# Kernel optimization log

Measured on AMD Instinct MI355X. Metric: run time of the kernel, lower is better.

## Reference

```python
import jax, jax.numpy as jnp
import numpy as np

D_MODEL = 512
NHEAD = 8
HEAD_DIM = D_MODEL // NHEAD  # 64
ROTARY_DIM = HEAD_DIM        # rotary_dim defaults to head_dim
WINDOW = (127, 128)          # (left, right) sliding window, flash-attn convention
ROPE_BASE = 10000.0


def setup_inputs() -> dict:
    key = jax.random.key(0)
    k1, k2, k3, k4 = jax.random.split(key, 4)
    N, T = 4, 2048
    x = jax.random.normal(k1, (N, T, D_MODEL), dtype=jnp.float32)
    # Wqkv: Linear(d_model, 3*d_model, bias=False) -> weight [3*D, D]
    Wqkv_w = jax.random.normal(k2, (3 * D_MODEL, D_MODEL), dtype=jnp.float32) * (D_MODEL ** -0.5)
    # out_proj: Linear(d_model, d_model, bias=True)
    out_w = jax.random.normal(k3, (D_MODEL, D_MODEL), dtype=jnp.float32) * (D_MODEL ** -0.5)
    out_b = jax.random.normal(k4, (D_MODEL,), dtype=jnp.float32) * 0.01
    return {"x": x, "Wqkv_w": Wqkv_w, "out_w": out_w, "out_b": out_b}


def _rope_cos_sin(T, dtype):
    # flash-attn RotaryEmbedding: inv_freq over even indices of rotary_dim
    inv_freq = 1.0 / (ROPE_BASE ** (jnp.arange(0, ROTARY_DIM, 2, dtype=jnp.float32) / ROTARY_DIM))
    t = jnp.arange(T, dtype=jnp.float32)
    freqs = jnp.outer(t, inv_freq)  # [T, ROTARY_DIM//2]
    return jnp.cos(freqs).astype(dtype), jnp.sin(freqs).astype(dtype)


def _apply_rotary(x, cos, sin):
    # non-interleaved (rotate halves); x: [N, T, H, hd], rotary over first ROTARY_DIM dims
    r, rest = x[..., :ROTARY_DIM], x[..., ROTARY_DIM:]
    half = ROTARY_DIM // 2
    x1, x2 = r[..., :half], r[..., half:]
    c = cos[None, :, None, :]  # [1, T, 1, half]
    s = sin[None, :, None, :]
    rotated = jnp.concatenate([x1 * c - x2 * s, x2 * c + x1 * s], axis=-1)
    return jnp.concatenate([rotated, rest], axis=-1) if rest.shape[-1] else rotated


def reference(x, Wqkv_w, out_w, out_b):
    N, T, D = x.shape
    qkv = jnp.einsum('ntd,ed->nte', x, Wqkv_w).reshape(N, T, 3, NHEAD, HEAD_DIM)
    q, k, v = qkv[:, :, 0], qkv[:, :, 1], qkv[:, :, 2]  # each [N, T, H, hd]
    cos, sin = _rope_cos_sin(T, x.dtype)
    q = _apply_rotary(q, cos, sin)
    k = _apply_rotary(k, cos, sin)
    scale = HEAD_DIM ** -0.5
    scores = jnp.einsum('nthd,nshd->nhts', q, k) * scale  # [N, H, T, T]
    # sliding window: query i attends key j iff i - left <= j <= i + right
    i = jnp.arange(T)[:, None]
    j = jnp.arange(T)[None, :]
    mask = (j >= i - WINDOW[0]) & (j <= i + WINDOW[1])  # [T, T]
    scores = jnp.where(mask[None, None], scores, jnp.finfo(scores.dtype).min)
    attn = jax.nn.softmax(scores, axis=-1)
    ctx = jnp.einsum('nhts,nshd->nthd', attn, v).reshape(N, T, D)
    return jnp.einsum('ntd,ed->nte', ctx, out_w) + out_b
```

## Files before the change

kernel.cpp:

```cpp
#include <hip/hip_runtime.h>
#include <math.h>

#define TSEQ 2048
#define NB 4
#define DM 512
#define NH 8
#define HD 64

typedef _Float16 half8 __attribute__((ext_vector_type(8)));
typedef _Float16 half4 __attribute__((ext_vector_type(4)));
typedef float floatx4 __attribute__((ext_vector_type(4)));


#define WS_END_U16 2916352

__global__ void prep(const float* __restrict__ x, const float* __restrict__ wqkv,
                     const float* __restrict__ ow, char* __restrict__ ws) {
  for (int i = blockIdx.x * 256 + threadIdx.x; i < WS_END_U16; i += 2048 * 256) {
    if (i < 524288) {
      const float4 a = ((const float4*)x)[2 * i];
      const float4 b = ((const float4*)x)[2 * i + 1];
      half8 h;
      h[0] = (_Float16)a.x; h[1] = (_Float16)a.y; h[2] = (_Float16)a.z; h[3] = (_Float16)a.w;
      h[4] = (_Float16)b.x; h[5] = (_Float16)b.y; h[6] = (_Float16)b.z; h[7] = (_Float16)b.w;
      *(half8*)(ws + (size_t)i * 16) = h;
    } else if (i >= 540672 && i < 638976) {
      const int o = i - 540672;
      const float4 a = ((const float4*)wqkv)[2 * o];
      const float4 b = ((const float4*)wqkv)[2 * o + 1];
      half8 h;
      h[0] = (_Float16)a.x; h[1] = (_Float16)a.y; h[2] = (_Float16)a.z; h[3] = (_Float16)a.w;
      h[4] = (_Float16)b.x; h[5] = (_Float16)b.y; h[6] = (_Float16)b.z; h[7] = (_Float16)b.w;
      *(half8*)(ws + (size_t)i * 16) = h;
    } else if (i >= 655360 && i < 688128) {
      const int o = i - 655360;
      const float4 a = ((const float4*)ow)[2 * o];
      const float4 b = ((const float4*)ow)[2 * o + 1];
      half8 h;
      h[0] = (_Float16)a.x; h[1] = (_Float16)a.y; h[2] = (_Float16)a.z; h[3] = (_Float16)a.w;
      h[4] = (_Float16)b.x; h[5] = (_Float16)b.y; h[6] = (_Float16)b.z; h[7] = (_Float16)b.w;
      *(half8*)(ws + (size_t)i * 16) = h;
    } else if (i >= 2883584) {
      const int u = i - 2883584;
      float4 o4;
      {
        const int id = 2 * u, t = id >> 5, fi = id & 31;
        const float invf = powf(10000.0f, -(float)(2 * fi) * (1.0f / 64.0f));
        float s, c; sincosf((float)t * invf, &s, &c);
        o4.x = c; o4.y = s;
      }
      {
        const int id = 2 * u + 1, t = id >> 5, fi = id & 31;
        const float invf = powf(10000.0f, -(float)(2 * fi) * (1.0f / 64.0f));
        float s, c; sincosf((float)t * invf, &s, &c);
        o4.z = c; o4.w = s;
      }
      ((float4*)(ws + 46137344))[u] = o4;
    } else {
      ((float4*)ws)[i] = make_float4(0.f, 0.f, 0.f, 0.f);
    }
  }
}

__global__ __launch_bounds__(256) void qkv_gemm_mfma(
    const _Float16* __restrict__ A, const _Float16* __restrict__ B,
    const float2* __restrict__ rope,
    _Float16* __restrict__ qb, _Float16* __restrict__ kb, _Float16* __restrict__ vT)
{
  __shared__ _Float16 As[128 * 40];
  __shared__ _Float16 Bs[128 * 40];
  const int tid = threadIdx.x;
  const int wv = tid >> 6, lane = tid & 63, quad = lane >> 4, col = lane & 15;
  const int wm = wv >> 1, we = wv & 1;
  const int m0 = blockIdx.x << 7, c0 = blockIdx.y << 7;
  const int sr = tid >> 1, sc = (tid & 1) << 4;
  const _Float16* ap = &A[(size_t)(m0 + sr) * DM + sc];
  const _Float16* bp = &B[(size_t)(c0 + sr) * DM + sc];
  floatx4 acc[4][4] = {};
  for (int k0 = 0; k0 < DM; k0 += 32) {
    const half8 a0 = *(const half8*)(ap + k0);
    const half8 a1 = *(const half8*)(ap + k0 + 8);
    const half8 b0 = *(const half8*)(bp + k0);
    const half8 b1 = *(const half8*)(bp + k0 + 8);
    __syncthreads();
    *(half8*)&As[sr * 40 + sc] = a0;
    *(half8*)&As[sr * 40 + sc + 8] = a1;
    *(half8*)&Bs[sr * 40 + sc] = b0;
    *(half8*)&Bs[sr * 40 + sc + 8] = b1;
    __syncthreads();
    half8 af[4], bf[4];
#pragma unroll
    for (int mt = 0; mt < 4; mt++)
      af[mt] = *(const half8*)&As[(wm * 64 + mt * 16 + col) * 40 + quad * 8];
#pragma unroll
    for (int et = 0; et < 4; et++)
      bf[et] = *(const half8*)&Bs[(we * 64 + et * 16 + col) * 40 + quad * 8];
#pragma unroll
    for (int mt = 0; mt < 4; mt++)
#pragma unroll
      for (int et = 0; et < 4; et++)
        acc[mt][et] = __builtin_amdgcn_mfma_f32_16x16x32_f16(af[mt], bf[et], acc[mt][et], 0, 0, 0);
  }
  const int eidx = (c0 >> 6) + we;
  const int three = eidx >> 3, h = eidx & 7;
  const int mbase = m0 + wm * 64 + quad * 4;
  if (three == 2) {
#pragma unroll
    for (int mt = 0; mt < 4; mt++) {
      const int m = mbase + mt * 16;
      const int n = m >> 11, t = m & 2047;
#pragma unroll
      for (int et = 0; et < 4; et++) {
        const int dh = et * 16 + col;
        half4 hv;
#pragma unroll
        for (int r = 0; r < 4; r++) hv[r] = (_Float16)acc[mt][et][r];
        *(half4*)&vT[(size_t)(n * NH + h) * HD * TSEQ + (size_t)dh * TSEQ + t] = hv;
      }
    }
  } else {
    _Float16* dst = three ? kb : qb;
    const float scl = three ? 1.0f : 0.125f;
#pragma unroll
    for (int mt = 0; mt < 4; mt++)
#pragma unroll
      for (int r = 0; r < 4; r++) {
        const int m = mbase + mt * 16 + r;
        const int n = m >> 11, t = m & 2047;
#pragma unroll
        for (int et = 0; et < 4; et++) {
          const int i = ((et & 1) << 4) + col;
          const float2 cs = rope[t * 32 + i];
          const float v = acc[mt][et][r];
          const float v2 = acc[mt][et ^ 2][r];
          const float o = (et < 2) ? (v * cs.x - v2 * cs.y) : (v * cs.x + v2 * cs.y);
          dst[((size_t)(n * NH + h) * TSEQ + t) * HD + et * 16 + col] = (_Float16)(o * scl);
        }
      }
  }
}

__global__ __launch_bounds__(256, 4) void attn_win_mfma(
    const _Float16* __restrict__ qb, const _Float16* __restrict__ kb,
    const _Float16* __restrict__ vT, _Float16* __restrict__ ctx)
{
  __shared__ __align__(16) char smem[36864];
  _Float16* Ks = (_Float16*)smem;
  _Float16* Vt = (_Float16*)(smem + 9216);
  _Float16* Ps = (_Float16*)(smem + 18432);
  _Float16* Osh = (_Float16*)(smem + 27648);

  const int tid = threadIdx.x;
  const int wv = tid >> 6;
  const int lane = tid & 63;
  const int quad = lane >> 4;
  const int col = lane & 15;
  const int nh = blockIdx.y;
  const int q0 = blockIdx.x << 6;
  const _Float16* qp = qb + (size_t)nh * TSEQ * HD;
  const _Float16* kp = kb + (size_t)nh * TSEQ * HD;
  const _Float16* vp = vT + (size_t)nh * HD * TSEQ;

  const int i_row = (wv << 4) + col;
  const int ig = q0 + i_row;
  const half8 qf0 = *(const half8*)&qp[(size_t)ig * HD + (quad << 3)];
  const half8 qf1 = *(const half8*)&qp[(size_t)ig * HD + 32 + (quad << 3)];

  float m_i = -1e30f, l_i = 0.0f;
  floatx4 accO[4] = {};

  const int kt0 = max(0, q0 - 127) >> 6;
  const int kt1 = min(TSEQ - 1, q0 + 191) >> 6;
  const int kr = tid >> 2, kc = (tid & 3) << 4;
  const int vd = tid >> 2, vc = (tid & 3) << 4;
  for (int kt = kt0; kt <= kt1; kt++) {
    const int j0 = kt << 6;
    const half8 k0_ = *(const half8*)&kp[(size_t)(j0 + kr) * HD + kc];
    const half8 k1_ = *(const half8*)&kp[(size_t)(j0 + kr) * HD + kc + 8];
    const half8 v0_ = *(const half8*)&vp[(size_t)vd * TSEQ + j0 + vc];
    const half8 v1_ = *(const half8*)&vp[(size_t)vd * TSEQ + j0 + vc + 8];
    __syncthreads();
    *(half8*)&Ks[kr * 72 + kc] = k0_;
    *(half8*)&Ks[kr * 72 + kc + 8] = k1_;
    *(half8*)&Vt[vd * 72 + vc] = v0_;
    *(half8*)&Vt[vd * 72 + vc + 8] = v1_;
    __syncthreads();

    floatx4 S[4];
#pragma unroll
    for (int js = 0; js < 4; js++) {
      const half8 a0 = *(const half8*)&Ks[((js << 4) + col) * 72 + (quad << 3)];
      const half8 a1 = *(const half8*)&Ks[((js << 4) + col) * 72 + 32 + (quad << 3)];
      floatx4 c = {0.f, 0.f, 0.f, 0.f};
      c = __builtin_amdgcn_mfma_f32_16x16x32_f16(a0, qf0, c, 0, 0, 0);
      c = __builtin_amdgcn_mfma_f32_16x16x32_f16(a1, qf1, c, 0, 0, 0);
      S[js] = c;
    }
    float mx = -1e30f;
#pragma unroll
    for (int js = 0; js < 4; js++)
#pragma unroll
      for (int r = 0; r < 4; r++) {
        const int jg = j0 + (js << 4) + (quad << 2) + r;
        const bool valid = (jg >= ig - 127) && (jg <= ig + 128);
        const float s = valid ? S[js][r] : -INFINITY;
        S[js][r] = s;
        mx = fmaxf(mx, s);
      }
    mx = fmaxf(mx, __shfl_xor(mx, 16, 64));
    mx = fmaxf(mx, __shfl_xor(mx, 32, 64));
    const float m_new = fmaxf(m_i, mx);
    const float alpha = __expf(m_i - m_new);
    float lsum = 0.f;
#pragma unroll
    for (int js = 0; js < 4; js++) {
      half4 ph;
#pragma unroll
      for (int r = 0; r < 4; r++) {
        const float p = __expf(S[js][r] - m_new);
        lsum += p;
        ph[r] = (_Float16)p;
      }
      *(half4*)&Ps[i_row * 72 + (js << 4) + (quad << 2)] = ph;
    }
    lsum += __shfl_xor(lsum, 16, 64);
    lsum += __shfl_xor(lsum, 32, 64);
    l_i = l_i * alpha + lsum;
    m_i = m_new;
    float a4[4];
#pragma unroll
    for (int r = 0; r < 4; r++) a4[r] = __shfl(alpha, (quad << 2) + r, 64);
#pragma unroll
    for (int d4 = 0; d4 < 4; d4++)
#pragma unroll
      for (int r = 0; r < 4; r++) accO[d4][r] *= a4[r];
    __syncthreads();
    const half8 pa0 = *(const half8*)&Ps[i_row * 72 + (quad << 3)];
    const half8 pa1 = *(const half8*)&Ps[i_row * 72 + 32 + (quad << 3)];
#pragma unroll
    for (int d4 = 0; d4 < 4; d4++) {
      const half8 vb0 = *(const half8*)&Vt[((d4 << 4) + col) * 72 + (quad << 3)];
      const half8 vb1 = *(const half8*)&Vt[((d4 << 4) + col) * 72 + 32 + (quad << 3)];
      accO[d4] = __builtin_amdgcn_mfma_f32_16x16x32_f16(pa0, vb0, accO[d4], 0, 0, 0);
      accO[d4] = __builtin_amdgcn_mfma_f32_16x16x32_f16(pa1, vb1, accO[d4], 0, 0, 0);
    }
  }
  {
    const float linv = 1.0f / l_i;
    float l4[4];
#pragma unroll
    for (int r = 0; r < 4; r++) l4[r] = __shfl(linv, (quad << 2) + r, 64);
#pragma unroll
    for (int d4 = 0; d4 < 4; d4++)
#pragma unroll
      for (int r = 0; r < 4; r++)
        Osh[((wv << 4) + (quad << 2) + r) * 72 + (d4 << 4) + col] = (_Float16)(accO[d4][r] * l4[r]);
  }
  __syncthreads();
  {
    const int n = nh >> 3, h = nh & 7;
    const int oi = tid >> 2, oc = (tid & 3) << 4;
    _Float16* dst = &ctx[((size_t)n * TSEQ + q0 + oi) * DM + h * HD + oc];
    *(half8*)&dst[0] = *(const half8*)&Osh[oi * 72 + oc];
    *(half8*)&dst[8] = *(const half8*)&Osh[oi * 72 + oc + 8];
  }
}

__global__ __launch_bounds__(256) void out_gemm_mfma(
    const _Float16* __restrict__ A, const _Float16* __restrict__ B,
    const float* __restrict__ bias, float* __restrict__ out)
{
  __shared__ _Float16 As[128 * 40];
  __shared__ _Float16 Bs[64 * 40];
  const int tid = threadIdx.x;
  const int wv = tid >> 6, lane = tid & 63, quad = lane >> 4, col = lane & 15;
  const int wm = wv >> 1, we = wv & 1;
  const int m0 = blockIdx.x << 7, c0 = blockIdx.y << 6;
  const int sr = tid >> 1, sc = (tid & 1) << 4;
  const int br = tid >> 2, bc = (tid & 3) << 3;
  const _Float16* ap = &A[(size_t)(m0 + sr) * DM + sc];
  const _Float16* bp = &B[(size_t)(c0 + br) * DM + bc];
  floatx4 acc[4][2] = {};
  for (int k0 = 0; k0 < DM; k0 += 32) {
    const half8 a0 = *(const half8*)(ap + k0);
    const half8 a1 = *(const half8*)(ap + k0 + 8);
    const half8 b0 = *(const half8*)(bp + k0);
    __syncthreads();
    *(half8*)&As[sr * 40 + sc] = a0;
    *(half8*)&As[sr * 40 + sc + 8] = a1;
    *(half8*)&Bs[br * 40 + bc] = b0;
    __syncthreads();
    half8 af[4], bf[2];
#pragma unroll
    for (int mt = 0; mt < 4; mt++)
      af[mt] = *(const half8*)&As[(wm * 64 + mt * 16 + col) * 40 + quad * 8];
#pragma unroll
    for (int et = 0; et < 2; et++)
      bf[et] = *(const half8*)&Bs[(we * 32 + et * 16 + col) * 40 + quad * 8];
#pragma unroll
    for (int mt = 0; mt < 4; mt++)
#pragma unroll
      for (int et = 0; et < 2; et++)
        acc[mt][et] = __builtin_amdgcn_mfma_f32_16x16x32_f16(af[mt], bf[et], acc[mt][et], 0, 0, 0);
  }
  float bb[2];
#pragma unroll
  for (int et = 0; et < 2; et++) bb[et] = bias[c0 + we * 32 + et * 16 + col];
  const int mbase = m0 + wm * 64 + quad * 4;
#pragma unroll
  for (int mt = 0; mt < 4; mt++)
#pragma unroll
    for (int r = 0; r < 4; r++) {
      const int m = mbase + mt * 16 + r;
#pragma unroll
      for (int et = 0; et < 2; et++)
        out[(size_t)m * DM + c0 + we * 32 + et * 16 + col] = acc[mt][et][r] + bb[et];
    }
}

extern "C" void kernel_launch(void* const* d_in, const int* in_sizes, int n_in,
                              void* d_out, int out_size, void* d_ws, size_t ws_size,
                              hipStream_t stream) {
  const float* x    = (const float*)d_in[0];
  const float* wqkv = (const float*)d_in[1];
  const float* ow   = (const float*)d_in[2];
  const float* ob   = (const float*)d_in[3];
  char* ws = (char*)d_ws;
  _Float16* xh    = (_Float16*)(ws);
  _Float16* wqkvh = (_Float16*)(ws + 8650752);
  _Float16* owh   = (_Float16*)(ws + 10485760);
  _Float16* qbuf  = (_Float16*)(ws + 11534336);
  _Float16* kbuf  = (_Float16*)(ws + 20971520);
  _Float16* vTb   = (_Float16*)(ws + 29360128);
  _Float16* ctxh  = (_Float16*)(ws + 37748736);
  float2*   rope  = (float2*)  (ws + 46137344);

  prep<<<2048, 256, 0, stream>>>(x, wqkv, ow, ws);
  qkv_gemm_mfma<<<dim3(64, 12), 256, 0, stream>>>(xh, wqkvh, rope, qbuf, kbuf, vTb);
  attn_win_mfma<<<dim3(32, 32), 256, 0, stream>>>(qbuf, kbuf, vTb, ctxh);
  out_gemm_mfma<<<dim3(64, 8), 256, 0, stream>>>(ctxh, owh, ob, (float*)d_out);
}
```

Before: 139.2 us.

## Use 128-wide key tiles with fixed three-iteration loop in windowed attention

The attention kernel now processes keys in 128-wide tiles aligned to 128, always looping over three tiles with clamped loads, instead of 64-wide tiles spanning the window. This halves the number of barrier-separated iterations and online-softmax rescales, and drops the barrier between P writes and P reads because each wave reads only its own rows. In exchange LDS grows to 52KB, occupancy bound drops to 3 blocks, and aligned tiles cover more masked-out keys than before.

```diff
diff --git a/kernel.cpp b/kernel.cpp
--- a/kernel.cpp
+++ b/kernel.cpp
@@ -140,15 +140,15 @@
   }
 }
 
-__global__ __launch_bounds__(256, 4) void attn_win_mfma(
+__global__ __launch_bounds__(256, 3) void attn_win_mfma(
     const _Float16* __restrict__ qb, const _Float16* __restrict__ kb,
     const _Float16* __restrict__ vT, _Float16* __restrict__ ctx)
 {
-  __shared__ __align__(16) char smem[36864];
+  __shared__ __align__(16) char smem[53248];
   _Float16* Ks = (_Float16*)smem;
-  _Float16* Vt = (_Float16*)(smem + 9216);
-  _Float16* Ps = (_Float16*)(smem + 18432);
-  _Float16* Osh = (_Float16*)(smem + 27648);
+  _Float16* Vt = (_Float16*)(smem + 18432);
+  _Float16* Ps = (_Float16*)(smem + 35840);
+  _Float16* Osh = (_Float16*)smem;
 
   const int tid = threadIdx.x;
   const int wv = tid >> 6;
@@ -169,26 +169,34 @@
   float m_i = -1e30f, l_i = 0.0f;
   floatx4 accO[4] = {};
 
-  const int kt0 = max(0, q0 - 127) >> 6;
-  const int kt1 = min(TSEQ - 1, q0 + 191) >> 6;
-  const int kr = tid >> 2, kc = (tid & 3) << 4;
-  const int vd = tid >> 2, vc = (tid & 3) << 4;
-  for (int kt = kt0; kt <= kt1; kt++) {
-    const int j0 = kt << 6;
-    const half8 k0_ = *(const half8*)&kp[(size_t)(j0 + kr) * HD + kc];
-    const half8 k1_ = *(const half8*)&kp[(size_t)(j0 + kr) * HD + kc + 8];
-    const half8 v0_ = *(const half8*)&vp[(size_t)vd * TSEQ + j0 + vc];
-    const half8 v1_ = *(const half8*)&vp[(size_t)vd * TSEQ + j0 + vc + 8];
-    __syncthreads();
-    *(half8*)&Ks[kr * 72 + kc] = k0_;
-    *(half8*)&Ks[kr * 72 + kc + 8] = k1_;
-    *(half8*)&Vt[vd * 72 + vc] = v0_;
-    *(half8*)&Vt[vd * 72 + vc + 8] = v1_;
-    __syncthreads();
-
-    floatx4 S[4];
-#pragma unroll
-    for (int js = 0; js < 4; js++) {
+  const int kr = tid >> 1, kc = (tid & 1) << 5;
+  const int vd = tid >> 2, vc = (tid & 3) << 5;
+  const int jb0 = (q0 & ~127) - 128;
+  for (int it = 0; it < 3; it++) {
+    const int jb = jb0 + (it << 7);
+    if (jb + 128 <= 0 || jb >= TSEQ) continue;
+    const int jrc = min(max(jb + kr, 0), TSEQ - 1);
+    half8 kreg[4], vreg[4];
+#pragma unroll
+    for (int c = 0; c < 4; c++)
+      kreg[c] = *(const half8*)&kp[(size_t)jrc * HD + kc + (c << 3)];
+#pragma unroll
+    for (int c = 0; c < 4; c++) {
+      const int jv = min(max(jb + vc + (c << 3), 0), TSEQ - 8);
+      vreg[c] = *(const half8*)&vp[(size_t)vd * TSEQ + jv];
+    }
+    __syncthreads();
+#pragma unroll
+    for (int c = 0; c < 4; c++)
+      *(half8*)&Ks[kr * 72 + kc + (c << 3)] = kreg[c];
+#pragma unroll
+    for (int c = 0; c < 4; c++)
+      *(half8*)&Vt[vd * 136 + vc + (c << 3)] = vreg[c];
+    __syncthreads();
+
+    floatx4 S[8];
+#pragma unroll
+    for (int js = 0; js < 8; js++) {
       const half8 a0 = *(const half8*)&Ks[((js << 4) + col) * 72 + (quad << 3)];
       const half8 a1 = *(const half8*)&Ks[((js << 4) + col) * 72 + 32 + (quad << 3)];
       floatx4 c = {0.f, 0.f, 0.f, 0.f};
@@ -196,14 +204,14 @@
       c = __builtin_amdgcn_mfma_f32_16x16x32_f16(a1, qf1, c, 0, 0, 0);
       S[js] = c;
     }
+    const int lo = max(ig - 127, 0), hi = min(ig + 128, TSEQ - 1);
     float mx = -1e30f;
 #pragma unroll
-    for (int js = 0; js < 4; js++)
+    for (int js = 0; js < 8; js++)
 #pragma unroll
       for (int r = 0; r < 4; r++) {
-        const int jg = j0 + (js << 4) + (quad << 2) + r;
-        const bool valid = (jg >= ig - 127) && (jg <= ig + 128);
-        const float s = valid ? S[js][r] : -INFINITY;
+        const int jg = jb + (js << 4) + (quad << 2) + r;
+        const float s = (jg >= lo && jg <= hi) ? S[js][r] : -INFINITY;
         S[js][r] = s;
         mx = fmaxf(mx, s);
       }
@@ -213,7 +221,7 @@
     const float alpha = __expf(m_i - m_new);
     float lsum = 0.f;
 #pragma unroll
-    for (int js = 0; js < 4; js++) {
+    for (int js = 0; js < 8; js++) {
       half4 ph;
 #pragma unroll
       for (int r = 0; r < 4; r++) {
@@ -221,7 +229,7 @@
         lsum += p;
         ph[r] = (_Float16)p;
       }
-      *(half4*)&Ps[i_row * 72 + (js << 4) + (quad << 2)] = ph;
+      *(half4*)&Ps[i_row * 136 + (js << 4) + (quad << 2)] = ph;
     }
     lsum += __shfl_xor(lsum, 16, 64);
     lsum += __shfl_xor(lsum, 32, 64);
@@ -234,17 +242,17 @@
     for (int d4 = 0; d4 < 4; d4++)
 #pragma unroll
       for (int r = 0; r < 4; r++) accO[d4][r] *= a4[r];
-    __syncthreads();
-    const half8 pa0 = *(const half8*)&Ps[i_row * 72 + (quad << 3)];
-    const half8 pa1 = *(const half8*)&Ps[i_row * 72 + 32 + (quad << 3)];
-#pragma unroll
-    for (int d4 = 0; d4 < 4; d4++) {
-      const half8 vb0 = *(const half8*)&Vt[((d4 << 4) + col) * 72 + (quad << 3)];
-      const half8 vb1 = *(const half8*)&Vt[((d4 << 4) + col) * 72 + 32 + (quad << 3)];
-      accO[d4] = __builtin_amdgcn_mfma_f32_16x16x32_f16(pa0, vb0, accO[d4], 0, 0, 0);
-      accO[d4] = __builtin_amdgcn_mfma_f32_16x16x32_f16(pa1, vb1, accO[d4], 0, 0, 0);
-    }
-  }
+#pragma unroll
+    for (int c = 0; c < 4; c++) {
+      const half8 pa = *(const half8*)&Ps[i_row * 136 + (c << 5) + (quad << 3)];
+#pragma unroll
+      for (int d4 = 0; d4 < 4; d4++) {
+        const half8 vbf = *(const half8*)&Vt[((d4 << 4) + col) * 136 + (c << 5) + (quad << 3)];
+        accO[d4] = __builtin_amdgcn_mfma_f32_16x16x32_f16(pa, vbf, accO[d4], 0, 0, 0);
+      }
+    }
+  }
+  __syncthreads();
   {
     const float linv = 1.0f / l_i;
     float l4[4];
```

Measured after the change: 146.5 us. 5.3% more time.
